# Kernel tuning notes

Hardware: AMD Instinct MI355X
Metric: run time of the kernel (lower is better)

## Reference

```python
import jax, jax.numpy as jnp
import numpy as np

HEADS = 8

def _grid_edges(H, W):
    # 4-neighbor grid adjacency, built at trace time (static), faithful to the torch double loop
    N = H * W
    idx = np.arange(N).reshape(H, W)
    e = np.zeros((N, N), np.float32)
    a, b = idx[1:, :].ravel(), idx[:-1, :].ravel()
    e[a, b] = 1.0; e[b, a] = 1.0
    a, b = idx[:, 1:].ravel(), idx[:, :-1].ravel()
    e[a, b] = 1.0; e[b, a] = 1.0
    return jnp.asarray(e)

def _layernorm(x, g, b, eps=1e-5):
    m = x.mean(-1, keepdims=True)
    v = x.var(-1, keepdims=True)
    return (x - m) / jnp.sqrt(v + eps) * g + b

def _gat(nodes, edges, W, b, rel):
    # nodes: [N,B,E]; W: [4,E,E] (q,k,v,out); rel: [HEADS]
    N, B, E = nodes.shape
    hd = E // HEADS
    q = (nodes @ W[0].T + b[0]).reshape(N, B, HEADS, hd)
    k = (nodes @ W[1].T + b[1]).reshape(N, B, HEADS, hd)
    v = (nodes @ W[2].T + b[2]).reshape(N, B, HEADS, hd)
    s = jnp.einsum('ibhd,jbhd->hbij', q, k) / float(np.sqrt(hd))
    s = s + edges[None, None] * rel[:, None, None, None]  # per-head edge relation bias
    a = jax.nn.softmax(s, axis=1)  # faithful to source: softmax over dim=1 (batch axis)
    o = jnp.einsum('hbij,jbhd->ibhd', a, v).reshape(N, B, E)
    return o @ W[3].T + b[3]

def _mha(q_in, kv_in, W, b):
    # standard nn.MultiheadAttention (eval, no dropout); seq-first [L,B,E]
    L, B, E = q_in.shape
    S = kv_in.shape[0]
    hd = E // HEADS
    q = (q_in @ W[0].T + b[0]).reshape(L, B, HEADS, hd)
    k = (kv_in @ W[1].T + b[1]).reshape(S, B, HEADS, hd)
    v = (kv_in @ W[2].T + b[2]).reshape(S, B, HEADS, hd)
    s = jnp.einsum('ibhd,jbhd->hbij', q, k) / float(np.sqrt(hd))
    a = jax.nn.softmax(s, axis=-1)
    o = jnp.einsum('hbij,jbhd->ibhd', a, v).reshape(L, B, E)
    return o @ W[3].T + b[3]

def reference(x, gat_W, gat_b, gat_rel, cross_W, cross_b, ln_g, ln_b):
    B, C, H, W = x.shape
    P = H // 4
    # global nodes: avg_pool2d(kernel=4) then flatten to [P*P, B, C]
    g = x.reshape(B, C, P, 4, P, 4).mean(axis=(3, 5))
    global_nodes = g.reshape(B, C, P * P).transpose(2, 0, 1)
    global_edges = jnp.ones((P * P, P * P), x.dtype)
    local_nodes = x.reshape(B, C, H * W).transpose(2, 0, 1)  # [HW,B,C]
    local_edges = _grid_edges(H, W)
    g_out = _gat(global_nodes, global_edges, gat_W[0], gat_b[0], gat_rel[0])
    g_out = _layernorm(g_out + global_nodes, ln_g[0], ln_b[0])
    l_out = _gat(local_nodes, local_edges, gat_W[1], gat_b[1], gat_rel[1])
    l_out = _layernorm(l_out + local_nodes, ln_g[1], ln_b[1])
    # nearest upsample x4 of global output back to HxW
    g_map = g_out.transpose(1, 2, 0).reshape(B, C, P, P)
    g_up = jnp.repeat(jnp.repeat(g_map, 4, axis=2), 4, axis=3)
    g_up = g_up.reshape(B, C, H * W).transpose(2, 0, 1)
    c_out = _mha(l_out, g_up, cross_W, cross_b)
    c_out = _layernorm(c_out + l_out, ln_g[2], ln_b[2])
    return c_out.transpose(1, 2, 0).reshape(B, C, H, W)

def setup_inputs() -> dict:
    key = jax.random.key(0)
    ks = jax.random.split(key, 6)
    B, C, H, W = 2, 256, 40, 40
    E = C
    sc = 0.02
    return {
        "x": jax.random.normal(ks[0], (B, C, H, W), jnp.float32),
        "gat_W": jax.random.normal(ks[1], (2, 4, E, E), jnp.float32) * sc,
        "gat_b": jax.random.normal(ks[2], (2, 4, E), jnp.float32) * sc,
        "gat_rel": jax.random.normal(ks[3], (2, HEADS), jnp.float32),
        "cross_W": jax.random.normal(ks[4], (4, E, E), jnp.float32) * sc,
        "cross_b": jax.random.normal(ks[5], (4, E), jnp.float32) * sc,
        "ln_g": jnp.ones((3, E), jnp.float32),
        "ln_b": jnp.zeros((3, E), jnp.float32),
    }
```

## Files before the change

kernel.cpp:

```cpp
#include <hip/hip_runtime.h>
#include <math.h>

#define NLOC 1600
#define NGLO 100

typedef unsigned short u16;
typedef short s16x8 __attribute__((ext_vector_type(8)));
typedef float f32x4 __attribute__((ext_vector_type(4)));

__device__ __forceinline__ short f2bf(float f) {
    unsigned u = __float_as_uint(f);
    u += 0x7fffu + ((u >> 16) & 1u);
    return (short)(u >> 16);
}
__device__ __forceinline__ float bf2f(u16 h) {
    return __uint_as_float(((unsigned)h) << 16);
}

__device__ __forceinline__ void gemm_core(int lane, const u16* __restrict__ A,
                                          const u16* __restrict__ W,
                                          int M, int m0, int n0, f32x4 acc[2][4]) {
    int c = lane & 15, qd = lane >> 4;
#pragma unroll
    for (int mi = 0; mi < 2; ++mi)
#pragma unroll
        for (int ni = 0; ni < 4; ++ni) acc[mi][ni] = (f32x4){0.f, 0.f, 0.f, 0.f};
#pragma unroll 2
    for (int kc = 0; kc < 8; ++kc) {
        int ko = kc * 32 + qd * 8;
        s16x8 af[2], bf[4];
#pragma unroll
        for (int mi = 0; mi < 2; ++mi) {
            int row = m0 + mi * 16 + c;
            s16x8 zz = {};
            af[mi] = (row < M) ? *(const s16x8*)(A + (size_t)row * 256 + ko) : zz;
        }
#pragma unroll
        for (int ni = 0; ni < 4; ++ni)
            bf[ni] = *(const s16x8*)(W + (size_t)(n0 + ni * 16 + c) * 256 + ko);
#pragma unroll
        for (int mi = 0; mi < 2; ++mi)
#pragma unroll
            for (int ni = 0; ni < 4; ++ni)
                acc[mi][ni] = __builtin_amdgcn_mfma_f32_16x16x32_bf16(af[mi], bf[ni],
                                                                      acc[mi][ni], 0, 0, 0);
    }
}

__device__ __forceinline__ void ep_row(int lane, f32x4 acc[2][4],
                                       const float* __restrict__ bias,
                                       u16* __restrict__ C, int M, int m0, int n0) {
    int c = lane & 15, qd = lane >> 4;
#pragma unroll
    for (int mi = 0; mi < 2; ++mi)
#pragma unroll
        for (int r = 0; r < 4; ++r) {
            int row = m0 + mi * 16 + 4 * qd + r;
            if (row < M) {
#pragma unroll
                for (int ni = 0; ni < 4; ++ni) {
                    int col = n0 + ni * 16 + c;
                    C[(size_t)row * 256 + col] = (u16)f2bf(acc[mi][ni][r] + bias[col]);
                }
            }
        }
}

__device__ __forceinline__ void ep_vt(int lane, f32x4 acc[2][4],
                                      const float* __restrict__ bias,
                                      u16* __restrict__ vt, int Npad,
                                      int M, int m0, int n0, float* sum) {
    int c = lane & 15, qd = lane >> 4;
    float s[4] = {0.f, 0.f, 0.f, 0.f};
#pragma unroll
    for (int mi = 0; mi < 2; ++mi)
#pragma unroll
        for (int r = 0; r < 4; ++r) {
            int row = m0 + mi * 16 + 4 * qd + r;
            if (row < M) {
                int n = row >> 1, b = row & 1;
#pragma unroll
                for (int ni = 0; ni < 4; ++ni) {
                    int col = n0 + ni * 16 + c;
                    float val = acc[mi][ni][r] + bias[col];
                    vt[(size_t)(b * 256 + col) * Npad + n] = (u16)f2bf(val);
                    if (b) s[ni] += val;
                }
            }
        }
    if (sum) {
#pragma unroll
        for (int ni = 0; ni < 4; ++ni)
            atomicAdd(&sum[n0 + ni * 16 + c], s[ni]);
    }
}

template <int MODE>
__device__ __forceinline__ void gemmln_block(int tid, const u16* __restrict__ A,
                                             const u16* __restrict__ W,
                                             const float* __restrict__ bias,
                                             const float* __restrict__ R,
                                             const float* __restrict__ g,
                                             const float* __restrict__ bb,
                                             float* fout, u16* bfout, float* dout,
                                             int M, int m0) {
    int w = tid >> 6, lane = tid & 63;
    int c = lane & 15, qd = lane >> 4;
    int n0 = w * 64;

    f32x4 acc[4] = {};
#pragma unroll 2
    for (int kc = 0; kc < 8; ++kc) {
        int ko = kc * 32 + qd * 8;
        int row = m0 + c;
        s16x8 zz = {};
        s16x8 af = (row < M) ? *(const s16x8*)(A + (size_t)row * 256 + ko) : zz;
#pragma unroll
        for (int ni = 0; ni < 4; ++ni) {
            s16x8 bf = *(const s16x8*)(W + (size_t)(n0 + ni * 16 + c) * 256 + ko);
            acc[ni] = __builtin_amdgcn_mfma_f32_16x16x32_bf16(af, bf, acc[ni], 0, 0, 0);
        }
    }

    __shared__ float ps1[4][16], ps2[4][16];
    float v[4][4];
#pragma unroll
    for (int r = 0; r < 4; ++r) {
        int row = m0 + 4 * qd + r;
        bool ok = (row < M);
        float s1 = 0.f, s2 = 0.f;
#pragma unroll
        for (int ni = 0; ni < 4; ++ni) {
            int col = n0 + ni * 16 + c;
            float val = acc[ni][r] + bias[col] + (ok ? R[(size_t)row * 256 + col] : 0.f);
            v[r][ni] = val;
            s1 += val; s2 += val * val;
        }
        s1 += __shfl_xor(s1, 1); s2 += __shfl_xor(s2, 1);
        s1 += __shfl_xor(s1, 2); s2 += __shfl_xor(s2, 2);
        s1 += __shfl_xor(s1, 4); s2 += __shfl_xor(s2, 4);
        s1 += __shfl_xor(s1, 8); s2 += __shfl_xor(s2, 8);
        if (c == 0) { ps1[w][4 * qd + r] = s1; ps2[w][4 * qd + r] = s2; }
    }
    __syncthreads();

    if (MODE == 0) {
#pragma unroll
        for (int r = 0; r < 4; ++r) {
            int lr = 4 * qd + r;
            int row = m0 + lr;
            if (row >= M) continue;
            float s1 = ps1[0][lr] + ps1[1][lr] + ps1[2][lr] + ps1[3][lr];
            float s2 = ps2[0][lr] + ps2[1][lr] + ps2[2][lr] + ps2[3][lr];
            float mean = s1 * (1.f / 256.f);
            float var  = s2 * (1.f / 256.f) - mean * mean;
            float rstd = rsqrtf(var + 1e-5f);
#pragma unroll
            for (int ni = 0; ni < 4; ++ni) {
                int col = n0 + ni * 16 + c;
                float y = (v[r][ni] - mean) * rstd * g[col] + bb[col];
                fout[(size_t)row * 256 + col] = y;
                bfout[(size_t)row * 256 + col] = (u16)f2bf(y);
            }
        }
    } else {
        __shared__ float ytile[2][8][256];
#pragma unroll
        for (int r = 0; r < 4; ++r) {
            int lr = 4 * qd + r;
            float s1 = ps1[0][lr] + ps1[1][lr] + ps1[2][lr] + ps1[3][lr];
            float s2 = ps2[0][lr] + ps2[1][lr] + ps2[2][lr] + ps2[3][lr];
            float mean = s1 * (1.f / 256.f);
            float var  = s2 * (1.f / 256.f) - mean * mean;
            float rstd = rsqrtf(var + 1e-5f);
#pragma unroll
            for (int ni = 0; ni < 4; ++ni) {
                int col = n0 + ni * 16 + c;
                ytile[lr & 1][lr >> 1][col] = (v[r][ni] - mean) * rstd * g[col] + bb[col];
            }
        }
        __syncthreads();
#pragma unroll
        for (int pp = tid; pp < 512; pp += 256) {
            int b = pp >> 8, col = pp & 255;
            float4 y0, y1;
            y0.x = ytile[b][0][col]; y0.y = ytile[b][1][col];
            y0.z = ytile[b][2][col]; y0.w = ytile[b][3][col];
            y1.x = ytile[b][4][col]; y1.y = ytile[b][5][col];
            y1.z = ytile[b][6][col]; y1.w = ytile[b][7][col];
            size_t o = ((size_t)(b * 256 + col)) * 1600 + (m0 >> 1);
            *(float4*)(dout + o)     = y0;
            *(float4*)(dout + o + 4) = y1;
        }
    }
}

__global__ __launch_bounds__(256) void k_prep(const float* __restrict__ gw,
                                              const float* __restrict__ cw,
                                              u16* __restrict__ gwb,
                                              u16* __restrict__ cwb,
                                              const float* __restrict__ x,
                                              float* __restrict__ nodes,
                                              u16* __restrict__ nodesb,
                                              float* __restrict__ gn,
                                              u16* __restrict__ gnb,
                                              float* __restrict__ sv1,
                                              u16* __restrict__ gvt,
                                              u16* __restrict__ cvt) {
    int bx = blockIdx.x;
    int tid = threadIdx.x;
    if (bx < 768) {
        int t = bx * 256 + tid;
        const float* src; u16* dst; int idx;
        if (t < 131072) { src = gw; dst = gwb; idx = t; }
        else            { src = cw; dst = cwb; idx = t - 131072; }
        float4 v = ((const float4*)src)[idx];
        ushort4 o;
        o.x = (u16)f2bf(v.x); o.y = (u16)f2bf(v.y);
        o.z = (u16)f2bf(v.z); o.w = (u16)f2bf(v.w);
        ((ushort4*)dst)[idx] = o;
    } else if (bx < 1568) {
        __shared__ float tile[32][33];
        int tt = bx - 768;
        int cb = tt / 100, rem = tt - cb * 100;
        int nb = rem >> 1, b = rem & 1;
        int c0 = cb * 32, n0t = nb * 32;
        int tx = tid & 31, ty = tid >> 5;
#pragma unroll
        for (int k2 = 0; k2 < 4; ++k2) {
            int cc = c0 + ty + k2 * 8;
            tile[ty + k2 * 8][tx] = x[((size_t)(b * 256 + cc)) * 1600 + n0t + tx];
        }
        __syncthreads();
#pragma unroll
        for (int k2 = 0; k2 < 4; ++k2) {
            int n = n0t + ty + k2 * 8;
            float val = tile[tx][ty + k2 * 8];
            size_t o = ((size_t)(n * 2 + b)) * 256 + c0 + tx;
            nodes[o] = val;
            nodesb[o] = (u16)f2bf(val);
        }
    } else if (bx < 1768) {
        int pt = bx - 1568;
        int b = pt & 1, n = pt >> 1;
        int cc = tid;
        int pr = n / 10, qqc = n - pr * 10;
        const float* xp = x + ((size_t)(b * 256 + cc)) * 1600 + (pr * 4) * 40 + qqc * 4;
        float s = 0.f;
#pragma unroll
        for (int dy = 0; dy < 4; ++dy)
#pragma unroll
            for (int dx = 0; dx < 4; ++dx)
                s += xp[dy * 40 + dx];
        s *= (1.f / 16.f);
        size_t t = (size_t)pt * 256 + cc;
        gn[t] = s;
        gnb[t] = (u16)f2bf(s);
    } else if (bx == 1768) {
        sv1[tid] = 0.f;
        sv1[tid + 256] = 0.f;
    } else if (bx == 1769) {
        for (int e2 = tid; e2 < 512; e2 += 256)
            for (int n = 100; n < 128; ++n) gvt[(size_t)e2 * 128 + n] = 0;
    } else {
        for (int e2 = tid; e2 < 512; e2 += 256)
            for (int n = 100; n < 128; ++n) cvt[(size_t)e2 * 128 + n] = 0;
    }
}

__global__ __launch_bounds__(64) void k_qkv(const u16* __restrict__ nodesb,
                                            const u16* __restrict__ gnb,
                                            const u16* __restrict__ W1b,
                                            const u16* __restrict__ W0b,
                                            const float* __restrict__ b1,
                                            const float* __restrict__ b0,
                                            u16* __restrict__ qbuf,
                                            u16* __restrict__ kbuf,
                                            u16* __restrict__ vtb,
                                            u16* __restrict__ gqb,
                                            u16* __restrict__ gkb,
                                            u16* __restrict__ gvt,
                                            float* __restrict__ sv1l,
                                            float* __restrict__ sv1g) {
    int lane = threadIdx.x;
    int bx = blockIdx.x, z = blockIdx.z;
    int n0 = blockIdx.y * 64;
    f32x4 acc[2][4];
    if (bx < 100) {
        int m0 = bx * 32;
        gemm_core(lane, nodesb, W1b + (size_t)z * 65536, 3200, m0, n0, acc);
        const float* bias = b1 + z * 256;
        if (z == 0)      ep_row(lane, acc, bias, qbuf, 3200, m0, n0);
        else if (z == 1) ep_row(lane, acc, bias, kbuf, 3200, m0, n0);
        else             ep_vt(lane, acc, bias, vtb, 1600, 3200, m0, n0, sv1l);
    } else {
        int m0 = (bx - 100) * 32;
        gemm_core(lane, gnb, W0b + (size_t)z * 65536, 200, m0, n0, acc);
        const float* bias = b0 + z * 256;
        if (z == 0)      ep_row(lane, acc, bias, gqb, 200, m0, n0);
        else if (z == 1) ep_row(lane, acc, bias, gkb, 200, m0, n0);
        else             ep_vt(lane, acc, bias, gvt, 128, 200, m0, n0, sv1g);
    }
}

__global__ __launch_bounds__(256) void k_attn(
    const u16* __restrict__ qb, const u16* __restrict__ kb,
    const u16* __restrict__ vt, float* __restrict__ pO, float* __restrict__ pT,
    const u16* __restrict__ gqb, const u16* __restrict__ gkb,
    const u16* __restrict__ gvt, const float* __restrict__ sv1g,
    u16* __restrict__ gattb)
{
    __shared__ u16 ks[2][32][40];
    __shared__ u16 vs[2][32][40];
    __shared__ short At4[4][16][40];

    int tid = threadIdx.x;
    int w = tid >> 6, lane = tid & 63;
    int c = lane & 15, qd = lane >> 4;
    int bx = blockIdx.x;

    if (bx < 800) {
        int q4 = bx & 3;
        int hic = bx >> 2;
        int ic = hic % 25, h = hic / 25;
        int hb = h * 32;
        int i0 = ic * 64 + w * 16;
        int jb0 = q4 * 13, jbe = (jb0 + 13 < 50) ? jb0 + 13 : 50;

        const u16* qp = qb + ((size_t)(i0 + c) * 2) * 256 + hb + qd * 8;
        s16x8 qf0 = *(const s16x8*)qp;
        s16x8 qf1 = *(const s16x8*)(qp + 256);
#pragma unroll
        for (int z = 0; z < 8; ++z) qf0[z] ^= (short)0x8000;

        f32x4 o0[2] = {}, t1[2] = {};

        int srow = tid >> 2, part = tid & 3;
        int sjl = srow >> 1, sb = srow & 1;
        int vb_ = srow >> 5, vd = srow & 31;

        for (int jb = jb0; jb < jbe; ++jb) {
            int j0 = jb * 32;
            __syncthreads();
            {
                s16x8 kv = *(const s16x8*)(kb + (size_t)(j0 + sjl) * 512 + sb * 256 + hb + part * 8);
                *(s16x8*)&ks[sb][sjl][part * 8] = kv;
                s16x8 vv = *(const s16x8*)(vt + (size_t)(vb_ * 256 + hb + vd) * 1600 + j0 + part * 8);
                *(s16x8*)&vs[vb_][vd][part * 8] = vv;
            }
            __syncthreads();

            s16x8 kf00 = *(const s16x8*)&ks[0][c][qd * 8];
            s16x8 kf10 = *(const s16x8*)&ks[1][c][qd * 8];
            s16x8 kf01 = *(const s16x8*)&ks[0][16 + c][qd * 8];
            s16x8 kf11 = *(const s16x8*)&ks[1][16 + c][qd * 8];

            f32x4 z4 = {};
            f32x4 sd0 = __builtin_amdgcn_mfma_f32_16x16x32_bf16(qf0, kf00, z4, 0, 0, 0);
            sd0       = __builtin_amdgcn_mfma_f32_16x16x32_bf16(qf1, kf10, sd0, 0, 0, 0);
            f32x4 sd1 = __builtin_amdgcn_mfma_f32_16x16x32_bf16(qf0, kf01, z4, 0, 0, 0);
            sd1       = __builtin_amdgcn_mfma_f32_16x16x32_bf16(qf1, kf11, sd1, 0, 0, 0);
#pragma unroll
            for (int r = 0; r < 4; ++r) {
                float e0v = __expf(sd0[r] * 0.17677669529663687f);
                At4[w][4 * qd + r][c]      = f2bf(__builtin_amdgcn_rcpf(1.f + e0v));
                float e1v = __expf(sd1[r] * 0.17677669529663687f);
                At4[w][4 * qd + r][16 + c] = f2bf(__builtin_amdgcn_rcpf(1.f + e1v));
            }
            asm volatile("s_waitcnt lgkmcnt(0)" ::: "memory");
            s16x8 af = *(const s16x8*)&At4[w][c][qd * 8];

            s16x8 vf00 = *(const s16x8*)&vs[0][c][qd * 8];
            s16x8 vf01 = *(const s16x8*)&vs[0][16 + c][qd * 8];
            s16x8 vf10 = *(const s16x8*)&vs[1][c][qd * 8];
            s16x8 vf11 = *(const s16x8*)&vs[1][16 + c][qd * 8];

            o0[0] = __builtin_amdgcn_mfma_f32_16x16x32_bf16(af, vf00, o0[0], 0, 0, 0);
            o0[1] = __builtin_amdgcn_mfma_f32_16x16x32_bf16(af, vf01, o0[1], 0, 0, 0);
            t1[0] = __builtin_amdgcn_mfma_f32_16x16x32_bf16(af, vf10, t1[0], 0, 0, 0);
            t1[1] = __builtin_amdgcn_mfma_f32_16x16x32_bf16(af, vf11, t1[1], 0, 0, 0);
        }

        size_t base = (size_t)q4 * 409600;
#pragma unroll
        for (int dh = 0; dh < 2; ++dh)
#pragma unroll
            for (int r = 0; r < 4; ++r) {
                size_t idx = base + (size_t)(i0 + 4 * qd + r) * 256 + hb + dh * 16 + c;
                pO[idx] = o0[dh][r];
                pT[idx] = t1[dh][r];
            }
    } else {
        int idx = (bx - 800) * 4 + w;
        int h = idx / 7, it = idx % 7;
        int i0 = it * 16;
        int hb = h * 32;

        s16x8 qf0 = {}, qf1 = {};
        int i = i0 + c;
        if (i < NGLO) {
            const u16* qp = gqb + ((size_t)i * 2) * 256 + hb + qd * 8;
            qf0 = *(const s16x8*)qp;
            qf1 = *(const s16x8*)(qp + 256);
        }
#pragma unroll
        for (int z = 0; z < 8; ++z) qf0[z] ^= (short)0x8000;

        f32x4 o0[2] = {}, t1[2] = {};

        for (int j0 = 0; j0 < NGLO; j0 += 32) {
            s16x8 kf[2][2], vf[2][2];
#pragma unroll
            for (int b = 0; b < 2; ++b)
#pragma unroll
                for (int js = 0; js < 2; ++js) {
                    int j = j0 + js * 16 + c;
                    s16x8 kv = {};
                    if (j < NGLO) kv = *(const s16x8*)(gkb + ((size_t)j * 2 + b) * 256 + hb + qd * 8);
                    kf[b][js] = kv;
                }
#pragma unroll
            for (int b = 0; b < 2; ++b)
#pragma unroll
                for (int dh = 0; dh < 2; ++dh)
                    vf[b][dh] = *(const s16x8*)(gvt + (size_t)(b * 256 + hb + dh * 16 + c) * 128
                                                + j0 + qd * 8);

            f32x4 z4 = {};
            f32x4 sd0 = __builtin_amdgcn_mfma_f32_16x16x32_bf16(qf0, kf[0][0], z4, 0, 0, 0);
            sd0       = __builtin_amdgcn_mfma_f32_16x16x32_bf16(qf1, kf[1][0], sd0, 0, 0, 0);
            f32x4 sd1 = __builtin_amdgcn_mfma_f32_16x16x32_bf16(qf0, kf[0][1], z4, 0, 0, 0);
            sd1       = __builtin_amdgcn_mfma_f32_16x16x32_bf16(qf1, kf[1][1], sd1, 0, 0, 0);
#pragma unroll
            for (int r = 0; r < 4; ++r) {
                float e0v = __expf(sd0[r] * 0.17677669529663687f);
                At4[w][4 * qd + r][c]      = f2bf(__builtin_amdgcn_rcpf(1.f + e0v));
                float e1v = __expf(sd1[r] * 0.17677669529663687f);
                At4[w][4 * qd + r][16 + c] = f2bf(__builtin_amdgcn_rcpf(1.f + e1v));
            }
            asm volatile("s_waitcnt lgkmcnt(0)" ::: "memory");
            s16x8 af = *(const s16x8*)&At4[w][c][qd * 8];
            o0[0] = __builtin_amdgcn_mfma_f32_16x16x32_bf16(af, vf[0][0], o0[0], 0, 0, 0);
            o0[1] = __builtin_amdgcn_mfma_f32_16x16x32_bf16(af, vf[0][1], o0[1], 0, 0, 0);
            t1[0] = __builtin_amdgcn_mfma_f32_16x16x32_bf16(af, vf[1][0], t1[0], 0, 0, 0);
            t1[1] = __builtin_amdgcn_mfma_f32_16x16x32_bf16(af, vf[1][1], t1[1], 0, 0, 0);
        }

#pragma unroll
        for (int dh = 0; dh < 2; ++dh) {
            float sv = sv1g[hb + dh * 16 + c];
#pragma unroll
            for (int r = 0; r < 4; ++r) {
                int ii = i0 + 4 * qd + r;
                if (ii < NGLO) {
                    size_t o = ((size_t)ii * 2) * 256 + hb + dh * 16 + c;
                    gattb[o]       = (u16)f2bf(o0[dh][r]);
                    gattb[o + 256] = (u16)f2bf(sv - t1[dh][r]);
                }
            }
        }
    }
}

__global__ __launch_bounds__(256) void k_combine_gproj(
    const float* __restrict__ pO, const float* __restrict__ pT,
    const float* __restrict__ sv1l, u16* __restrict__ attb,
    const u16* __restrict__ gattb, const u16* __restrict__ W0p,
    const float* __restrict__ b0p, const float* __restrict__ gn,
    const float* __restrict__ ln_g, const float* __restrict__ ln_b,
    float* __restrict__ gout, u16* __restrict__ goutb)
{
    int bx = blockIdx.x;
    if (bx < 400) {
        int t4 = (bx * 256 + threadIdx.x) * 4;
        int e = t4 & 255;
        int i = t4 >> 8;
        float4 o  = *(const float4*)(pO + t4);
        float4 tt = *(const float4*)(pT + t4);
#pragma unroll
        for (int q = 1; q < 4; ++q) {
            float4 a = *(const float4*)(pO + t4 + q * 409600);
            float4 b = *(const float4*)(pT + t4 + q * 409600);
            o.x += a.x; o.y += a.y; o.z += a.z; o.w += a.w;
            tt.x += b.x; tt.y += b.y; tt.z += b.z; tt.w += b.w;
        }
        float4 sv = *(const float4*)(sv1l + e);
        ushort4 w0, w1;
        w0.x = (u16)f2bf(o.x); w0.y = (u16)f2bf(o.y);
        w0.z = (u16)f2bf(o.z); w0.w = (u16)f2bf(o.w);
        w1.x = (u16)f2bf(sv.x - tt.x); w1.y = (u16)f2bf(sv.y - tt.y);
        w1.z = (u16)f2bf(sv.z - tt.z); w1.w = (u16)f2bf(sv.w - tt.w);
        *(ushort4*)(attb + (size_t)i * 512 + e)       = w0;
        *(ushort4*)(attb + (size_t)i * 512 + 256 + e) = w1;
    } else {
        gemmln_block<0>(threadIdx.x, gattb, W0p, b0p, gn, ln_g, ln_b,
                        gout, goutb, (float*)0, 200, (bx - 400) * 16);
    }
}

__global__ __launch_bounds__(256) void k_lproj_ckcv(
    const u16* __restrict__ attb, const u16* __restrict__ W1p,
    const float* __restrict__ b1p, const float* __restrict__ nodes,
    const float* __restrict__ ln_g1, const float* __restrict__ ln_b1,
    float* __restrict__ lout, u16* __restrict__ loutb,
    const u16* __restrict__ goutb, const u16* __restrict__ wckv,
    const float* __restrict__ bckv, u16* __restrict__ ckb,
    u16* __restrict__ cvt)
{
    int bx = blockIdx.x;
    if (bx < 200) {
        gemmln_block<0>(threadIdx.x, attb, W1p, b1p, nodes, ln_g1, ln_b1,
                        lout, loutb, (float*)0, 3200, bx * 16);
    } else {
        int w = threadIdx.x >> 6, lane = threadIdx.x & 63;
        int idx = (bx - 200) * 4 + w;
        if (idx < 56) {
            int z = idx / 28, rem = idx % 28;
            int m0 = (rem >> 2) * 32, n0 = (rem & 3) * 64;
            f32x4 acc[2][4];
            gemm_core(lane, goutb, wckv + (size_t)z * 65536, 200, m0, n0, acc);
            const float* bias = bckv + z * 256;
            if (z == 0) ep_row(lane, acc, bias, ckb, 200, m0, n0);
            else        ep_vt(lane, acc, bias, cvt, 128, 200, m0, n0, (float*)0);
        }
    }
}

__global__ __launch_bounds__(256) void k_cross(
    const u16* __restrict__ loutb, const u16* __restrict__ wcq,
    const float* __restrict__ bcq, const u16* __restrict__ kb,
    const u16* __restrict__ vt, u16* __restrict__ out)
{
    __shared__ short At[4][16][136];
    __shared__ short Aq[4][16][40];
    int w = threadIdx.x >> 6, lane = threadIdx.x & 63;
    int c  = lane & 15;
    int qd = lane >> 4;
    int idx = blockIdx.x * 4 + w;
    int it = idx % 100;
    int hb2 = idx / 100;
    int h = hb2 >> 1, b = hb2 & 1;
    int i0 = it * 16;
    int hb = h * 32;

    for (int z = lane; z < 16 * 24; z += 64)
        At[w][z / 24][112 + (z % 24)] = 0;

    f32x4 qacc[2] = {};
#pragma unroll 2
    for (int kc = 0; kc < 8; ++kc) {
        int ko = kc * 32 + qd * 8;
        s16x8 af = *(const s16x8*)(loutb + ((size_t)(i0 + c) * 2 + b) * 256 + ko);
#pragma unroll
        for (int ni = 0; ni < 2; ++ni) {
            s16x8 bf = *(const s16x8*)(wcq + (size_t)(hb + ni * 16 + c) * 256 + ko);
            qacc[ni] = __builtin_amdgcn_mfma_f32_16x16x32_bf16(af, bf, qacc[ni], 0, 0, 0);
        }
    }
#pragma unroll
    for (int ni = 0; ni < 2; ++ni)
#pragma unroll
        for (int r = 0; r < 4; ++r)
            Aq[w][4 * qd + r][ni * 16 + c] = f2bf(qacc[ni][r] + bcq[hb + ni * 16 + c]);
    asm volatile("s_waitcnt lgkmcnt(0)" ::: "memory");
    s16x8 qf = *(const s16x8*)&Aq[w][c][qd * 8];

    f32x4 s[7];
#pragma unroll
    for (int jt = 0; jt < 7; ++jt) {
        int j = jt * 16 + c;
        s16x8 kf = {};
        if (j < NGLO) kf = *(const s16x8*)(kb + ((size_t)j * 2 + b) * 256 + hb + qd * 8);
        f32x4 z4 = {};
        s[jt] = __builtin_amdgcn_mfma_f32_16x16x32_bf16(qf, kf, z4, 0, 0, 0);
    }
    if (c >= 4) {
#pragma unroll
        for (int r = 0; r < 4; ++r) s[6][r] = -1e30f;
    }
#pragma unroll
    for (int jt = 0; jt < 7; ++jt)
#pragma unroll
        for (int r = 0; r < 4; ++r) s[jt][r] *= 0.17677669529663687f;

    float l[4];
#pragma unroll
    for (int r = 0; r < 4; ++r) {
        float mm = s[0][r];
#pragma unroll
        for (int jt = 1; jt < 7; ++jt) mm = fmaxf(mm, s[jt][r]);
        mm = fmaxf(mm, __shfl_xor(mm, 1));
        mm = fmaxf(mm, __shfl_xor(mm, 2));
        mm = fmaxf(mm, __shfl_xor(mm, 4));
        mm = fmaxf(mm, __shfl_xor(mm, 8));
        float ll = 0.f;
#pragma unroll
        for (int jt = 0; jt < 7; ++jt) {
            float pv = __expf(s[jt][r] - mm);
            s[jt][r] = pv;
            ll += pv;
        }
        ll += __shfl_xor(ll, 1);
        ll += __shfl_xor(ll, 2);
        ll += __shfl_xor(ll, 4);
        ll += __shfl_xor(ll, 8);
        l[r] = ll;
    }
#pragma unroll
    for (int jt = 0; jt < 7; ++jt)
#pragma unroll
        for (int r = 0; r < 4; ++r)
            At[w][4 * qd + r][jt * 16 + c] = f2bf(s[jt][r]);
    asm volatile("s_waitcnt lgkmcnt(0)" ::: "memory");

    f32x4 o[2] = {};
#pragma unroll
    for (int kc = 0; kc < 4; ++kc) {
        s16x8 af = *(const s16x8*)&At[w][c][kc * 32 + qd * 8];
#pragma unroll
        for (int dh = 0; dh < 2; ++dh) {
            s16x8 vf = *(const s16x8*)(vt + (size_t)(b * 256 + hb + dh * 16 + c) * 128
                                       + kc * 32 + qd * 8);
            o[dh] = __builtin_amdgcn_mfma_f32_16x16x32_bf16(af, vf, o[dh], 0, 0, 0);
        }
    }
#pragma unroll
    for (int dh = 0; dh < 2; ++dh)
#pragma unroll
        for (int r = 0; r < 4; ++r) {
            int ii = i0 + 4 * qd + r;
            out[((size_t)ii * 2 + b) * 256 + hb + dh * 16 + c] = (u16)f2bf(o[dh][r] / l[r]);
        }
}

__global__ __launch_bounds__(256) void k_cproj(
    const u16* __restrict__ cattb, const u16* __restrict__ wcp,
    const float* __restrict__ bcp, const float* __restrict__ lout,
    const float* __restrict__ ln_g2, const float* __restrict__ ln_b2,
    float* __restrict__ dout)
{
    gemmln_block<1>(threadIdx.x, cattb, wcp, bcp, lout, ln_g2, ln_b2,
                    (float*)0, (u16*)0, dout, 3200, blockIdx.x * 16);
}

extern "C" void kernel_launch(void* const* d_in, const int* in_sizes, int n_in,
                              void* d_out, int out_size, void* d_ws, size_t ws_size,
                              hipStream_t stream) {
    const float* x        = (const float*)d_in[0];
    const float* gat_W    = (const float*)d_in[1];
    const float* gat_b    = (const float*)d_in[2];
    const float* cross_W  = (const float*)d_in[4];
    const float* cross_b  = (const float*)d_in[5];
    const float* ln_g     = (const float*)d_in[6];
    const float* ln_b     = (const float*)d_in[7];
    float* out = (float*)d_out;

    float* ws    = (float*)d_ws;
    float* nodes = ws;
    float* gn    = nodes + 819200;
    float* gout  = gn + 51200;
    float* lout  = gout + 51200;
    float* sv1l  = lout + 819200;
    float* sv1g  = sv1l + 256;
    float* pO    = sv1g + 256;
    float* pT    = pO + 1638400;

    u16* ub = (u16*)(pT + 1638400);
    u16* wgatb  = ub;            ub += 524288;
    u16* wcrsb  = ub;            ub += 262144;
    u16* nodesb = ub;            ub += 819200;
    u16* gnb    = ub;            ub += 51200;
    u16* qbuf   = ub;            ub += 819200;
    u16* kbuf   = ub;            ub += 819200;
    u16* vtb    = ub;            ub += 819200;
    u16* gqb    = ub;            ub += 51200;
    u16* gkb    = ub;            ub += 51200;
    u16* gvt    = ub;            ub += 65536;
    u16* gattb  = ub;            ub += 51200;
    u16* goutb  = ub;            ub += 51200;
    u16* attb   = ub;            ub += 819200;
    u16* loutb  = ub;            ub += 819200;
    u16* ckb    = ub;            ub += 51200;
    u16* cvt    = ub;            ub += 65536;
    u16* cattb  = kbuf;

    const u16* W0b = wgatb;
    const u16* W1b = wgatb + 4 * 65536;
    const float* b0 = gat_b;
    const float* b1 = gat_b + 4 * 256;

    k_prep<<<1771, 256, 0, stream>>>(gat_W, cross_W, wgatb, wcrsb,
                                     x, nodes, nodesb, gn, gnb, sv1l, gvt, cvt);
    k_qkv<<<dim3(107, 4, 3), 64, 0, stream>>>(nodesb, gnb, W1b, W0b, b1, b0,
                                              qbuf, kbuf, vtb, gqb, gkb, gvt,
                                              sv1l, sv1g);
    k_attn<<<814, 256, 0, stream>>>(qbuf, kbuf, vtb, pO, pT,
                                    gqb, gkb, gvt, sv1g, gattb);
    k_combine_gproj<<<413, 256, 0, stream>>>(pO, pT, sv1l, attb,
                                             gattb, W0b + 3 * 65536, b0 + 768, gn,
                                             ln_g, ln_b, gout, goutb);
    k_lproj_ckcv<<<214, 256, 0, stream>>>(attb, W1b + 3 * 65536, b1 + 768, nodes,
                                          ln_g + 256, ln_b + 256, lout, loutb,
                                          goutb, wcrsb + 65536, cross_b + 256,
                                          ckb, cvt);
    k_cross<<<400, 256, 0, stream>>>(loutb, wcrsb, cross_b, ckb, cvt, cattb);
    k_cproj<<<200, 256, 0, stream>>>(cattb, wcrsb + 3 * 65536, cross_b + 768, lout,
                                     ln_g + 512, ln_b + 512, out);
}
```

Before: 185.2 us.

## Use 16-row GEMM tiles with preloaded A, prefetched W, and LDS-staged V transpose

Shrinks the projection GEMM tiles from 32 to 16 rows, which doubles the grid for more parallelism. Each wave now preloads its whole A row fragment into registers and double-buffers the weight fragments across the k-loop. The V-transpose epilogue now stages results in LDS and writes 16-byte vector stores instead of scattered 2-byte stores. The cost is more register pressure and twice as many weight reads per output, since each weight tile is reused across fewer rows.

```diff
diff --git a/kernel.cpp b/kernel.cpp
--- a/kernel.cpp
+++ b/kernel.cpp
@@ -17,77 +17,87 @@
     return __uint_as_float(((unsigned)h) << 16);
 }
 
-__device__ __forceinline__ void gemm_core(int lane, const u16* __restrict__ A,
-                                          const u16* __restrict__ W,
-                                          int M, int m0, int n0, f32x4 acc[2][4]) {
+__device__ __forceinline__ void gemm16(int lane, const u16* __restrict__ A,
+                                       const u16* __restrict__ W,
+                                       int M, int m0, int n0, f32x4 acc[4]) {
     int c = lane & 15, qd = lane >> 4;
-#pragma unroll
-    for (int mi = 0; mi < 2; ++mi)
-#pragma unroll
-        for (int ni = 0; ni < 4; ++ni) acc[mi][ni] = (f32x4){0.f, 0.f, 0.f, 0.f};
-#pragma unroll 2
+    int arow = m0 + c;
+    bool aok = (arow < M);
+    const u16* ap = A + (size_t)arow * 256 + qd * 8;
+    s16x8 zz = {};
+    s16x8 afr[8];
+#pragma unroll
+    for (int kc = 0; kc < 8; ++kc)
+        afr[kc] = aok ? *(const s16x8*)(ap + kc * 32) : zz;
+    const u16* wp = W + (size_t)(n0 + c) * 256 + qd * 8;
+    s16x8 wcur[4], wnxt[4];
+#pragma unroll
+    for (int ni = 0; ni < 4; ++ni)
+        wcur[ni] = *(const s16x8*)(wp + (size_t)ni * 4096);
+#pragma unroll
+    for (int ni = 0; ni < 4; ++ni) acc[ni] = (f32x4){0.f, 0.f, 0.f, 0.f};
+#pragma unroll
     for (int kc = 0; kc < 8; ++kc) {
-        int ko = kc * 32 + qd * 8;
-        s16x8 af[2], bf[4];
-#pragma unroll
-        for (int mi = 0; mi < 2; ++mi) {
-            int row = m0 + mi * 16 + c;
-            s16x8 zz = {};
-            af[mi] = (row < M) ? *(const s16x8*)(A + (size_t)row * 256 + ko) : zz;
+        if (kc < 7) {
+#pragma unroll
+            for (int ni = 0; ni < 4; ++ni)
+                wnxt[ni] = *(const s16x8*)(wp + (size_t)ni * 4096 + (kc + 1) * 32);
         }
 #pragma unroll
         for (int ni = 0; ni < 4; ++ni)
-            bf[ni] = *(const s16x8*)(W + (size_t)(n0 + ni * 16 + c) * 256 + ko);
-#pragma unroll
-        for (int mi = 0; mi < 2; ++mi)
-#pragma unroll
-            for (int ni = 0; ni < 4; ++ni)
-                acc[mi][ni] = __builtin_amdgcn_mfma_f32_16x16x32_bf16(af[mi], bf[ni],
-                                                                      acc[mi][ni], 0, 0, 0);
-    }
-}
-
-__device__ __forceinline__ void ep_row(int lane, f32x4 acc[2][4],
-                                       const float* __restrict__ bias,
-                                       u16* __restrict__ C, int M, int m0, int n0) {
+            acc[ni] = __builtin_amdgcn_mfma_f32_16x16x32_bf16(afr[kc], wcur[ni],
+                                                              acc[ni], 0, 0, 0);
+        if (kc < 7) {
+#pragma unroll
+            for (int ni = 0; ni < 4; ++ni) wcur[ni] = wnxt[ni];
+        }
+    }
+}
+
+__device__ __forceinline__ void ep_row16(int lane, f32x4 acc[4],
+                                         const float* __restrict__ bias,
+                                         u16* __restrict__ C, int M, int m0, int n0) {
     int c = lane & 15, qd = lane >> 4;
 #pragma unroll
-    for (int mi = 0; mi < 2; ++mi)
-#pragma unroll
-        for (int r = 0; r < 4; ++r) {
-            int row = m0 + mi * 16 + 4 * qd + r;
-            if (row < M) {
-#pragma unroll
-                for (int ni = 0; ni < 4; ++ni) {
-                    int col = n0 + ni * 16 + c;
-                    C[(size_t)row * 256 + col] = (u16)f2bf(acc[mi][ni][r] + bias[col]);
-                }
+    for (int r = 0; r < 4; ++r) {
+        int row = m0 + 4 * qd + r;
+        if (row < M) {
+#pragma unroll
+            for (int ni = 0; ni < 4; ++ni) {
+                int col = n0 + ni * 16 + c;
+                C[(size_t)row * 256 + col] = (u16)f2bf(acc[ni][r] + bias[col]);
             }
         }
-}
-
-__device__ __forceinline__ void ep_vt(int lane, f32x4 acc[2][4],
-                                      const float* __restrict__ bias,
-                                      u16* __restrict__ vt, int Npad,
-                                      int M, int m0, int n0, float* sum) {
+    }
+}
+
+__device__ __forceinline__ void ep_vt16(int lane, u16* vtile, f32x4 acc[4],
+                                        const float* __restrict__ bias,
+                                        u16* __restrict__ vt, int Npad,
+                                        int M, int m0, int n0, float* sum) {
     int c = lane & 15, qd = lane >> 4;
     float s[4] = {0.f, 0.f, 0.f, 0.f};
 #pragma unroll
-    for (int mi = 0; mi < 2; ++mi)
-#pragma unroll
-        for (int r = 0; r < 4; ++r) {
-            int row = m0 + mi * 16 + 4 * qd + r;
-            if (row < M) {
-                int n = row >> 1, b = row & 1;
-#pragma unroll
-                for (int ni = 0; ni < 4; ++ni) {
-                    int col = n0 + ni * 16 + c;
-                    float val = acc[mi][ni][r] + bias[col];
-                    vt[(size_t)(b * 256 + col) * Npad + n] = (u16)f2bf(val);
-                    if (b) s[ni] += val;
-                }
-            }
-        }
+    for (int r = 0; r < 4; ++r) {
+        int row = m0 + 4 * qd + r;
+        int b = r & 1;
+        int n_loc = 2 * qd + (r >> 1);
+        bool ok = (row < M);
+#pragma unroll
+        for (int ni = 0; ni < 4; ++ni) {
+            int col = n0 + ni * 16 + c;
+            float val = ok ? (acc[ni][r] + bias[col]) : 0.f;
+            vtile[(b * 64 + ni * 16 + c) * 8 + n_loc] = (u16)f2bf(val);
+            if (b && ok) s[ni] += val;
+        }
+    }
+    asm volatile("s_waitcnt lgkmcnt(0)" ::: "memory");
+    int nst = m0 >> 1;
+#pragma unroll
+    for (int b2 = 0; b2 < 2; ++b2) {
+        s16x8 v0 = *(const s16x8*)(vtile + (b2 * 64 + lane) * 8);
+        *(s16x8*)(vt + (size_t)(b2 * 256 + n0 + lane) * Npad + nst) = v0;
+    }
     if (sum) {
 #pragma unroll
         for (int ni = 0; ni < 4; ++ni)
@@ -108,17 +118,34 @@
     int c = lane & 15, qd = lane >> 4;
     int n0 = w * 64;
 
+    int arow = m0 + c;
+    bool aok = (arow < M);
+    const u16* ap = A + (size_t)arow * 256 + qd * 8;
+    s16x8 zz = {};
+    s16x8 afr[8];
+#pragma unroll
+    for (int kc = 0; kc < 8; ++kc)
+        afr[kc] = aok ? *(const s16x8*)(ap + kc * 32) : zz;
+    const u16* wp = W + (size_t)(n0 + c) * 256 + qd * 8;
+    s16x8 wcur[4], wnxt[4];
+#pragma unroll
+    for (int ni = 0; ni < 4; ++ni)
+        wcur[ni] = *(const s16x8*)(wp + (size_t)ni * 4096);
     f32x4 acc[4] = {};
-#pragma unroll 2
+#pragma unroll
     for (int kc = 0; kc < 8; ++kc) {
-        int ko = kc * 32 + qd * 8;
-        int row = m0 + c;
-        s16x8 zz = {};
-        s16x8 af = (row < M) ? *(const s16x8*)(A + (size_t)row * 256 + ko) : zz;
-#pragma unroll
-        for (int ni = 0; ni < 4; ++ni) {
-            s16x8 bf = *(const s16x8*)(W + (size_t)(n0 + ni * 16 + c) * 256 + ko);
-            acc[ni] = __builtin_amdgcn_mfma_f32_16x16x32_bf16(af, bf, acc[ni], 0, 0, 0);
+        if (kc < 7) {
+#pragma unroll
+            for (int ni = 0; ni < 4; ++ni)
+                wnxt[ni] = *(const s16x8*)(wp + (size_t)ni * 4096 + (kc + 1) * 32);
+        }
+#pragma unroll
+        for (int ni = 0; ni < 4; ++ni)
+            acc[ni] = __builtin_amdgcn_mfma_f32_16x16x32_bf16(afr[kc], wcur[ni],
+                                                              acc[ni], 0, 0, 0);
+        if (kc < 7) {
+#pragma unroll
+            for (int ni = 0; ni < 4; ++ni) wcur[ni] = wnxt[ni];
         }
     }
 
@@ -282,24 +309,25 @@
                                             u16* __restrict__ gvt,
                                             float* __restrict__ sv1l,
                                             float* __restrict__ sv1g) {
+    __shared__ u16 vtile[2 * 64 * 8];
     int lane = threadIdx.x;
     int bx = blockIdx.x, z = blockIdx.z;
     int n0 = blockIdx.y * 64;
-    f32x4 acc[2][4];
-    if (bx < 100) {
-        int m0 = bx * 32;
-        gemm_core(lane, nodesb, W1b + (size_t)z * 65536, 3200, m0, n0, acc);
+    f32x4 acc[4];
+    if (bx < 200) {
+        int m0 = bx * 16;
+        gemm16(lane, nodesb, W1b + (size_t)z * 65536, 3200, m0, n0, acc);
         const float* bias = b1 + z * 256;
-        if (z == 0)      ep_row(lane, acc, bias, qbuf, 3200, m0, n0);
-        else if (z == 1) ep_row(lane, acc, bias, kbuf, 3200, m0, n0);
-        else             ep_vt(lane, acc, bias, vtb, 1600, 3200, m0, n0, sv1l);
+        if (z == 0)      ep_row16(lane, acc, bias, qbuf, 3200, m0, n0);
+        else if (z == 1) ep_row16(lane, acc, bias, kbuf, 3200, m0, n0);
+        else             ep_vt16(lane, vtile, acc, bias, vtb, 1600, 3200, m0, n0, sv1l);
     } else {
-        int m0 = (bx - 100) * 32;
-        gemm_core(lane, gnb, W0b + (size_t)z * 65536, 200, m0, n0, acc);
+        int m0 = (bx - 200) * 16;
+        gemm16(lane, gnb, W0b + (size_t)z * 65536, 200, m0, n0, acc);
         const float* bias = b0 + z * 256;
-        if (z == 0)      ep_row(lane, acc, bias, gqb, 200, m0, n0);
-        else if (z == 1) ep_row(lane, acc, bias, gkb, 200, m0, n0);
-        else             ep_vt(lane, acc, bias, gvt, 128, 200, m0, n0, sv1g);
+        if (z == 0)      ep_row16(lane, acc, bias, gqb, 200, m0, n0);
+        else if (z == 1) ep_row16(lane, acc, bias, gkb, 200, m0, n0);
+        else             ep_vt16(lane, vtile, acc, bias, gvt, 128, 200, m0, n0, sv1g);
     }
 }
 
@@ -507,6 +535,7 @@
     const float* __restrict__ bckv, u16* __restrict__ ckb,
     u16* __restrict__ cvt)
 {
+    __shared__ u16 vtile4[4][2 * 64 * 8];
     int bx = blockIdx.x;
     if (bx < 200) {
         gemmln_block<0>(threadIdx.x, attb, W1p, b1p, nodes, ln_g1, ln_b1,
@@ -514,14 +543,14 @@
     } else {
         int w = threadIdx.x >> 6, lane = threadIdx.x & 63;
         int idx = (bx - 200) * 4 + w;
-        if (idx < 56) {
-            int z = idx / 28, rem = idx % 28;
-            int m0 = (rem >> 2) * 32, n0 = (rem & 3) * 64;
-            f32x4 acc[2][4];
-            gemm_core(lane, goutb, wckv + (size_t)z * 65536, 200, m0, n0, acc);
+        if (idx < 104) {
+            int z = idx / 52, rem = idx % 52;
+            int m0 = (rem >> 2) * 16, n0 = (rem & 3) * 64;
+            f32x4 acc[4];
+            gemm16(lane, goutb, wckv + (size_t)z * 65536, 200, m0, n0, acc);
             const float* bias = bckv + z * 256;
-            if (z == 0) ep_row(lane, acc, bias, ckb, 200, m0, n0);
-            else        ep_vt(lane, acc, bias, cvt, 128, 200, m0, n0, (float*)0);
+            if (z == 0) ep_row16(lane, acc, bias, ckb, 200, m0, n0);
+            else        ep_vt16(lane, vtile4[w], acc, bias, cvt, 128, 200, m0, n0, (float*)0);
         }
     }
 }
@@ -546,15 +575,17 @@
     for (int z = lane; z < 16 * 24; z += 64)
         At[w][z / 24][112 + (z % 24)] = 0;
 
+    const u16* ap = loutb + ((size_t)(i0 + c) * 2 + b) * 256 + qd * 8;
+    s16x8 afr[8];
+#pragma unroll
+    for (int kc = 0; kc < 8; ++kc) afr[kc] = *(const s16x8*)(ap + kc * 32);
     f32x4 qacc[2] = {};
-#pragma unroll 2
+#pragma unroll
     for (int kc = 0; kc < 8; ++kc) {
-        int ko = kc * 32 + qd * 8;
-        s16x8 af = *(const s16x8*)(loutb + ((size_t)(i0 + c) * 2 + b) * 256 + ko);
 #pragma unroll
         for (int ni = 0; ni < 2; ++ni) {
-            s16x8 bf = *(const s16x8*)(wcq + (size_t)(hb + ni * 16 + c) * 256 + ko);
-            qacc[ni] = __builtin_amdgcn_mfma_f32_16x16x32_bf16(af, bf, qacc[ni], 0, 0, 0);
+            s16x8 bf = *(const s16x8*)(wcq + (size_t)(hb + ni * 16 + c) * 256 + kc * 32 + qd * 8);
+            qacc[ni] = __builtin_amdgcn_mfma_f32_16x16x32_bf16(afr[kc], bf, qacc[ni], 0, 0, 0);
         }
     }
 #pragma unroll
@@ -691,7 +722,7 @@
 
     k_prep<<<1771, 256, 0, stream>>>(gat_W, cross_W, wgatb, wcrsb,
                                      x, nodes, nodesb, gn, gnb, sv1l, gvt, cvt);
-    k_qkv<<<dim3(107, 4, 3), 64, 0, stream>>>(nodesb, gnb, W1b, W0b, b1, b0,
+    k_qkv<<<dim3(213, 4, 3), 64, 0, stream>>>(nodesb, gnb, W1b, W0b, b1, b0,
                                               qbuf, kbuf, vtb, gqb, gkb, gvt,
                                               sv1l, sv1g);
     k_attn<<<814, 256, 0, stream>>>(qbuf, kbuf, vtb, pO, pT,
@@ -699,7 +730,7 @@
     k_combine_gproj<<<413, 256, 0, stream>>>(pO, pT, sv1l, attb,
                                              gattb, W0b + 3 * 65536, b0 + 768, gn,
                                              ln_g, ln_b, gout, goutb);
-    k_lproj_ckcv<<<214, 256, 0, stream>>>(attb, W1b + 3 * 65536, b1 + 768, nodes,
+    k_lproj_ckcv<<<226, 256, 0, stream>>>(attb, W1b + 3 * 65536, b1 + 768, nodes,
                                           ln_g + 256, ln_b + 256, lout, loutb,
                                           goutb, wcrsb + 65536, cross_b + 256,
                                           ckb, cvt);
```

New measurement: 231.4 us. 1.25x slower.
